# Kernel tuning notes

Measured on AMD Instinct MI355X. Metric: run time of the kernel, lower is better.

## Reference

```python
import jax, jax.numpy as jnp
import numpy as np

D, H, S, T, NN, IN_CH, FEAT, SPA, OUT, NL, FF, E = 512, 8, 64, 32, 512, 32, 64, 32, 32, 4, 2048, 16384
NEG = 0.2  # leaky relu negative slope (GATv2 default and alpha)

def _ln(x, g, b):
    m = x.mean(-1, keepdims=True)
    v = ((x - m) ** 2).mean(-1, keepdims=True)
    return (x - m) / jnp.sqrt(v + 1e-5) * g + b

def _posenc(L):
    pos = jnp.arange(L, dtype=jnp.float32)[:, None]
    div = jnp.exp(-jnp.log(10000.0) * jnp.arange(0, D, 2, dtype=jnp.float32) / D)
    pe = jnp.zeros((L, D), jnp.float32)
    pe = pe.at[:, 0::2].set(jnp.sin(pos * div)).at[:, 1::2].set(jnp.cos(pos * div))
    return pe[:, None, :]  # (L,1,D), seq-first

def _mha(xq, xkv, wqkv, bqkv, wo, bo, mask=None):
    Lq, N, _ = xq.shape
    Lk = xkv.shape[0]
    dh = D // H
    wq, wk, wv = jnp.split(wqkv, 3, axis=1)
    bq, bk, bv = jnp.split(bqkv, 3)
    q = (xq @ wq + bq).reshape(Lq, N, H, dh)
    k = (xkv @ wk + bk).reshape(Lk, N, H, dh)
    v = (xkv @ wv + bv).reshape(Lk, N, H, dh)
    s = jnp.einsum('qnhd,knhd->nhqk', q, k) / jnp.sqrt(jnp.float32(dh))
    if mask is not None:
        s = s + mask
    a = jax.nn.softmax(s, -1)
    o = jnp.einsum('nhqk,knhd->qnhd', a, v).reshape(Lq, N, D)
    return o @ wo + bo

def _gatv2(x, wl, wr, bl, br, att, bias, e_src, e_dst):
    # GATv2: e_ij = a . leakyrelu(Wl x_j + Wr x_i); softmax over incoming edges of i; out_i = sum alpha_ij Wl x_j
    n = x.shape[0]
    h, c = att.shape
    xl = (x @ wl + bl).reshape(n, h, c)
    xr = (x @ wr + br).reshape(n, h, c)
    z = jax.nn.leaky_relu(xl[e_src] + xr[e_dst], NEG)   # (E,H,C)
    e = jnp.einsum('ehc,hc->eh', z, att)                # (E,H)
    m = jax.lax.stop_gradient(jax.ops.segment_max(e, e_dst, num_segments=n))
    ex = jnp.exp(e - m[e_dst])
    den = jax.ops.segment_sum(ex, e_dst, num_segments=n)
    alpha = ex / den[e_dst]
    out = jax.ops.segment_sum(alpha[..., None] * xl[e_src], e_dst, num_segments=n)
    return out.reshape(n, h * c) + bias

def _fwd(src, tgt, w_enc_in, b_enc_in, w_dec_in, b_dec_in, w_map, b_map,
         enc_qkv_w, enc_qkv_b, enc_out_w, enc_out_b, enc_ff1_w, enc_ff1_b, enc_ff2_w, enc_ff2_b,
         enc_ln1_g, enc_ln1_b, enc_ln2_g, enc_ln2_b, enc_fn_g, enc_fn_b,
         dec_sa_qkv_w, dec_sa_qkv_b, dec_sa_out_w, dec_sa_out_b,
         dec_ca_qkv_w, dec_ca_qkv_b, dec_ca_out_w, dec_ca_out_b,
         dec_ff1_w, dec_ff1_b, dec_ff2_w, dec_ff2_b,
         dec_ln1_g, dec_ln1_b, dec_ln2_g, dec_ln2_b, dec_ln3_g, dec_ln3_b, dec_fn_g, dec_fn_b,
         g1_wl, g1_wr, g1_bl, g1_br, g1_att, g1_bias,
         g2_wl, g2_wr, g2_bl, g2_br, g2_att, g2_bias,
         edge_index):
    # temporal transformer (eval mode, dropout off), seq-first (L, N, D)
    x = src @ w_enc_in + b_enc_in + _posenc(S)
    for i in range(NL):  # post-norm encoder, relu FFN (nn.TransformerEncoderLayer defaults)
        a = _mha(x, x, enc_qkv_w[i], enc_qkv_b[i], enc_out_w[i], enc_out_b[i])
        x = _ln(x + a, enc_ln1_g[i], enc_ln1_b[i])
        f = jax.nn.relu(x @ enc_ff1_w[i] + enc_ff1_b[i]) @ enc_ff2_w[i] + enc_ff2_b[i]
        x = _ln(x + f, enc_ln2_g[i], enc_ln2_b[i])
    mem = _ln(x, enc_fn_g, enc_fn_b)
    causal = jnp.triu(jnp.full((T, T), -1e9, jnp.float32), k=1)
    y = tgt @ w_dec_in + b_dec_in + _posenc(T)
    for i in range(NL):
        a = _mha(y, y, dec_sa_qkv_w[i], dec_sa_qkv_b[i], dec_sa_out_w[i], dec_sa_out_b[i], causal)
        y = _ln(y + a, dec_ln1_g[i], dec_ln1_b[i])
        a = _mha(y, mem, dec_ca_qkv_w[i], dec_ca_qkv_b[i], dec_ca_out_w[i], dec_ca_out_b[i])
        y = _ln(y + a, dec_ln2_g[i], dec_ln2_b[i])
        f = jax.nn.relu(y @ dec_ff1_w[i] + dec_ff1_b[i]) @ dec_ff2_w[i] + dec_ff2_b[i]
        y = _ln(y + f, dec_ln3_g[i], dec_ln3_b[i])
    y = _ln(y, dec_fn_g, dec_fn_b) @ w_map + b_map  # (T, N, FEAT)
    e_src, e_dst = edge_index[0], edge_index[1]
    def spatial(xt):  # two-layer GATv2 per time step, then elu (concat=True branch)
        h1 = _gatv2(xt, g1_wl, g1_wr, g1_bl, g1_br, g1_att, g1_bias, e_src, e_dst)
        h2 = _gatv2(h1, g2_wl, g2_wr, g2_bl, g2_br, g2_att, g2_bias, e_src, e_dst)
        return jax.nn.elu(h2)
    g = jax.vmap(spatial)(y)  # (T, N, H*OUT)
    return jax.nn.relu(g)


def setup_inputs():
    ks = iter(jax.random.split(jax.random.key(0), 100))
    def w(shape, s=0.05):
        return jax.random.normal(next(ks), shape, jnp.float32) * s
    inp = {}
    inp['src'] = jax.random.normal(next(ks), (S, NN, IN_CH), jnp.float32)
    inp['tgt'] = jax.random.normal(next(ks), (T, NN, FEAT), jnp.float32)
    inp['w_enc_in'] = w((IN_CH, D)); inp['b_enc_in'] = jnp.zeros((D,))
    inp['w_dec_in'] = w((FEAT, D)); inp['b_dec_in'] = jnp.zeros((D,))
    inp['w_map'] = w((D, FEAT)); inp['b_map'] = jnp.zeros((FEAT,))
    inp['enc_qkv_w'] = w((NL, D, 3 * D)); inp['enc_qkv_b'] = jnp.zeros((NL, 3 * D))
    inp['enc_out_w'] = w((NL, D, D)); inp['enc_out_b'] = jnp.zeros((NL, D))
    inp['enc_ff1_w'] = w((NL, D, FF)); inp['enc_ff1_b'] = jnp.zeros((NL, FF))
    inp['enc_ff2_w'] = w((NL, FF, D)); inp['enc_ff2_b'] = jnp.zeros((NL, D))
    inp['enc_ln1_g'] = jnp.ones((NL, D)); inp['enc_ln1_b'] = jnp.zeros((NL, D))
    inp['enc_ln2_g'] = jnp.ones((NL, D)); inp['enc_ln2_b'] = jnp.zeros((NL, D))
    inp['enc_fn_g'] = jnp.ones((D,)); inp['enc_fn_b'] = jnp.zeros((D,))
    inp['dec_sa_qkv_w'] = w((NL, D, 3 * D)); inp['dec_sa_qkv_b'] = jnp.zeros((NL, 3 * D))
    inp['dec_sa_out_w'] = w((NL, D, D)); inp['dec_sa_out_b'] = jnp.zeros((NL, D))
    inp['dec_ca_qkv_w'] = w((NL, D, 3 * D)); inp['dec_ca_qkv_b'] = jnp.zeros((NL, 3 * D))
    inp['dec_ca_out_w'] = w((NL, D, D)); inp['dec_ca_out_b'] = jnp.zeros((NL, D))
    inp['dec_ff1_w'] = w((NL, D, FF)); inp['dec_ff1_b'] = jnp.zeros((NL, FF))
    inp['dec_ff2_w'] = w((NL, FF, D)); inp['dec_ff2_b'] = jnp.zeros((NL, D))
    inp['dec_ln1_g'] = jnp.ones((NL, D)); inp['dec_ln1_b'] = jnp.zeros((NL, D))
    inp['dec_ln2_g'] = jnp.ones((NL, D)); inp['dec_ln2_b'] = jnp.zeros((NL, D))
    inp['dec_ln3_g'] = jnp.ones((NL, D)); inp['dec_ln3_b'] = jnp.zeros((NL, D))
    inp['dec_fn_g'] = jnp.ones((D,)); inp['dec_fn_b'] = jnp.zeros((D,))
    inp['g1_wl'] = w((FEAT, H * SPA)); inp['g1_wr'] = w((FEAT, H * SPA))
    inp['g1_bl'] = jnp.zeros((H * SPA,)); inp['g1_br'] = jnp.zeros((H * SPA,))
    inp['g1_att'] = w((H, SPA), 0.1); inp['g1_bias'] = jnp.zeros((H * SPA,))
    inp['g2_wl'] = w((H * SPA, H * OUT)); inp['g2_wr'] = w((H * SPA, H * OUT))
    inp['g2_bl'] = jnp.zeros((H * OUT,)); inp['g2_br'] = jnp.zeros((H * OUT,))
    inp['g2_att'] = w((H, OUT), 0.1); inp['g2_bias'] = jnp.zeros((H * OUT,))
    inp['edge_index'] = jax.random.randint(next(ks), (2, E), 0, NN)
    return inp


def reference(src, tgt, w_enc_in, b_enc_in, w_dec_in, b_dec_in, w_map, b_map,
              enc_qkv_w, enc_qkv_b, enc_out_w, enc_out_b, enc_ff1_w, enc_ff1_b, enc_ff2_w, enc_ff2_b,
              enc_ln1_g, enc_ln1_b, enc_ln2_g, enc_ln2_b, enc_fn_g, enc_fn_b,
              dec_sa_qkv_w, dec_sa_qkv_b, dec_sa_out_w, dec_sa_out_b,
              dec_ca_qkv_w, dec_ca_qkv_b, dec_ca_out_w, dec_ca_out_b,
              dec_ff1_w, dec_ff1_b, dec_ff2_w, dec_ff2_b,
              dec_ln1_g, dec_ln1_b, dec_ln2_g, dec_ln2_b, dec_ln3_g, dec_ln3_b, dec_fn_g, dec_fn_b,
              g1_wl, g1_wr, g1_bl, g1_br, g1_att, g1_bias,
              g2_wl, g2_wr, g2_bl, g2_br, g2_att, g2_bias,
              edge_index):
    return _fwd(src, tgt, w_enc_in, b_enc_in, w_dec_in, b_dec_in, w_map, b_map,
                enc_qkv_w, enc_qkv_b, enc_out_w, enc_out_b, enc_ff1_w, enc_ff1_b, enc_ff2_w, enc_ff2_b,
                enc_ln1_g, enc_ln1_b, enc_ln2_g, enc_ln2_b, enc_fn_g, enc_fn_b,
                dec_sa_qkv_w, dec_sa_qkv_b, dec_sa_out_w, dec_sa_out_b,
                dec_ca_qkv_w, dec_ca_qkv_b, dec_ca_out_w, dec_ca_out_b,
                dec_ff1_w, dec_ff1_b, dec_ff2_w, dec_ff2_b,
                dec_ln1_g, dec_ln1_b, dec_ln2_g, dec_ln2_b, dec_ln3_g, dec_ln3_b, dec_fn_g, dec_fn_b,
                g1_wl, g1_wr, g1_bl, g1_br, g1_att, g1_bias,
                g2_wl, g2_wr, g2_bl, g2_br, g2_att, g2_bias,
                edge_index)
```

## Files before the change

### kernel.cpp

```cpp
#include <hip/hip_runtime.h>
#include <hip/hip_bf16.h>

#define NHEAD 8
#define SLEN 64
#define TLEN 32
#define NNODE 512
#define NEDGE 16384
#define NLAYER 4

typedef __attribute__((ext_vector_type(8))) __bf16 bf16x8;
typedef __attribute__((ext_vector_type(4))) __bf16 bf16x4;
typedef __attribute__((ext_vector_type(4))) float  f32x4;

__device__ __forceinline__ void gload16(const void* g, void* l)
{
    __builtin_amdgcn_global_load_lds(
        (const __attribute__((address_space(1))) void*)g,
        (__attribute__((address_space(3))) void*)l, 16, 0, 0);
}

template<int BN>
__global__ __launch_bounds__(256) void gemm_bf16(
    const __bf16* __restrict__ A, int lda,
    const __bf16* __restrict__ Bt, int ldb,
    const float* __restrict__ bias,
    const __bf16* __restrict__ Res,
    float* __restrict__ Cf, __bf16* __restrict__ Cb, int ldc,
    int M, int N, int K, int outMode)
{
    constexpr int FM = (BN == 128) ? 4 : 2;
    __shared__ __bf16 As[128 * 64];
    __shared__ __bf16 Bs[BN * 64];
    const int tid  = threadIdx.x;
    const int wid  = tid >> 6;
    const int lane = tid & 63;
    const int wr = (BN == 128) ? (wid >> 1) : wid;
    const int wc = (BN == 128) ? (wid & 1) : 0;
    const int m0 = blockIdx.y * 128, n0 = blockIdx.x * BN;

    const int srow = wid * 8 + (lane >> 3);
    const int scol = (lane & 7) * 8;
    const int lr = lane & 15;
    const int kg = (lane >> 4) * 8;

    f32x4 acc[FM][4];
    #pragma unroll
    for (int m = 0; m < FM; ++m)
        #pragma unroll
        for (int n = 0; n < 4; ++n)
            acc[m][n] = (f32x4){0.0f, 0.0f, 0.0f, 0.0f};

    for (int k0 = 0; k0 < K; k0 += 64) {
        #pragma unroll
        for (int g = 0; g < 4; ++g) {
            const __bf16* ga = A + (size_t)(m0 + g * 32 + srow) * lda + k0 + scol;
            gload16(ga, &As[(g * 32 + wid * 8) * 64]);
        }
        #pragma unroll
        for (int g = 0; g < BN / 32; ++g) {
            const __bf16* gb = Bt + (size_t)(n0 + g * 32 + srow) * ldb + k0 + scol;
            gload16(gb, &Bs[(g * 32 + wid * 8) * 64]);
        }
        __syncthreads();
        #pragma unroll
        for (int kk = 0; kk < 64; kk += 32) {
            bf16x8 fa[FM], fb[4];
            #pragma unroll
            for (int m = 0; m < FM; ++m)
                fa[m] = *reinterpret_cast<const bf16x8*>(
                    &As[(wr * (16 * FM) + m * 16 + lr) * 64 + kk + kg]);
            #pragma unroll
            for (int n = 0; n < 4; ++n)
                fb[n] = *reinterpret_cast<const bf16x8*>(
                    &Bs[(wc * 64 + n * 16 + lr) * 64 + kk + kg]);
            #pragma unroll
            for (int m = 0; m < FM; ++m)
                #pragma unroll
                for (int n = 0; n < 4; ++n)
                    acc[m][n] = __builtin_amdgcn_mfma_f32_16x16x32_bf16(
                        fa[m], fb[n], acc[m][n], 0, 0, 0);
        }
        __syncthreads();
    }

    const int cr = (lane >> 4) * 4;
    const int cc = lane & 15;
    #pragma unroll
    for (int n = 0; n < 4; ++n) {
        const int gcol = n0 + wc * 64 + n * 16 + cc;
        const float bb = bias[gcol];
        #pragma unroll
        for (int m = 0; m < FM; ++m) {
            #pragma unroll
            for (int j = 0; j < 4; ++j) {
                const int grow = m0 + wr * (16 * FM) + m * 16 + cr + j;
                float v = acc[m][n][j] + bb;
                if (Res) v += (float)Res[(size_t)grow * ldc + gcol];
                if (outMode == 1 || outMode == 2) v = fmaxf(v, 0.0f);
                if (outMode >= 2) Cb[(size_t)grow * ldc + gcol] = (__bf16)v;
                else              Cf[(size_t)grow * ldc + gcol] = v;
            }
        }
    }
}

__global__ __launch_bounds__(256) void gemm_bias(
    const float* __restrict__ A, int lda,
    const float* __restrict__ B, int ldb,
    const float* __restrict__ bias,
    float* __restrict__ C, int ldc,
    int M, int N, int K, int relu)
{
    __shared__ float As[16][68];
    __shared__ float Bs[16][68];
    const int tid = threadIdx.x;
    const int tx = tid & 15, ty = tid >> 4;
    const int m0 = blockIdx.y * 64, n0 = blockIdx.x * 64;
    const int liA_m = tid >> 2;
    const int liA_k = (tid & 3) * 4;
    const int liB_n = (tid & 15) * 4;
    const int liB_k = tid >> 4;
    float acc[4][4] = {};
    for (int k0 = 0; k0 < K; k0 += 16) {
        float4 av = *reinterpret_cast<const float4*>(&A[(size_t)(m0 + liA_m) * lda + k0 + liA_k]);
        float4 bv = *reinterpret_cast<const float4*>(&B[(size_t)(k0 + liB_k) * ldb + n0 + liB_n]);
        As[liA_k + 0][liA_m] = av.x;
        As[liA_k + 1][liA_m] = av.y;
        As[liA_k + 2][liA_m] = av.z;
        As[liA_k + 3][liA_m] = av.w;
        *reinterpret_cast<float4*>(&Bs[liB_k][liB_n]) = bv;
        __syncthreads();
        #pragma unroll
        for (int kk = 0; kk < 16; ++kk) {
            float4 a4 = *reinterpret_cast<const float4*>(&As[kk][ty * 4]);
            float4 b4 = *reinterpret_cast<const float4*>(&Bs[kk][tx * 4]);
            float a[4] = {a4.x, a4.y, a4.z, a4.w};
            float b[4] = {b4.x, b4.y, b4.z, b4.w};
            #pragma unroll
            for (int i = 0; i < 4; ++i)
                #pragma unroll
                for (int j = 0; j < 4; ++j)
                    acc[i][j] += a[i] * b[j];
        }
        __syncthreads();
    }
    #pragma unroll
    for (int i = 0; i < 4; ++i) {
        const int m = m0 + ty * 4 + i;
        #pragma unroll
        for (int j = 0; j < 4; ++j) {
            const int n = n0 + tx * 4 + j;
            float v = acc[i][j] + bias[n];
            if (relu) v = fmaxf(v, 0.0f);
            C[(size_t)m * ldc + n] = v;
        }
    }
}

__global__ __launch_bounds__(256) void transpose_w(
    const float* __restrict__ in, __bf16* __restrict__ out, int K, int N)
{
    __shared__ __bf16 t[32][33];
    const int l = blockIdx.z;
    in  += (size_t)l * K * N;
    out += (size_t)l * K * N;
    const int k0 = blockIdx.y * 32, n0 = blockIdx.x * 32;
    const int tx = threadIdx.x & 31, ty = threadIdx.x >> 5;
    #pragma unroll
    for (int i = 0; i < 32; i += 8)
        t[ty + i][tx] = (__bf16)in[(size_t)(k0 + ty + i) * N + n0 + tx];
    __syncthreads();
    #pragma unroll
    for (int i = 0; i < 32; i += 8)
        out[(size_t)(n0 + ty + i) * K + k0 + tx] = t[tx][ty + i];
}

__global__ __launch_bounds__(256) void conv_bf16(
    const float* __restrict__ in, __bf16* __restrict__ out, int total4)
{
    const int i = blockIdx.x * 256 + threadIdx.x;
    if (i >= total4) return;
    const float4 v = *reinterpret_cast<const float4*>(&in[(size_t)i * 4]);
    bf16x4 w;
    w[0] = (__bf16)v.x; w[1] = (__bf16)v.y; w[2] = (__bf16)v.z; w[3] = (__bf16)v.w;
    *reinterpret_cast<bf16x4*>(&out[(size_t)i * 4]) = w;
}

__global__ __launch_bounds__(256) void permute_in(
    const float* __restrict__ in, float* __restrict__ out, int L, int CH, int total)
{
    const int idx = blockIdx.x * 256 + threadIdx.x;
    if (idx >= total) return;
    const int c = idx % CH;
    const int r = idx / CH;
    const int n = r & 511;
    const int l = r >> 9;
    out[((size_t)n * L + l) * CH + c] = in[idx];
}

__global__ __launch_bounds__(256) void permute_F(
    const __bf16* __restrict__ in, __bf16* __restrict__ out)
{
    const int idx = blockIdx.x * 256 + threadIdx.x;
    if (idx >= 16384 * 64) return;
    const int c = idx & 63;
    const int r = idx >> 6;
    const int n = r >> 5;
    const int t = r & 31;
    out[((size_t)(t * 512 + n)) * 64 + c] = in[idx];
}

template<int LQ, int LK, bool CAUSAL>
__global__ __launch_bounds__(64) void attn_mfma(
    const __bf16* __restrict__ Q, int ldq,
    const __bf16* __restrict__ Kp, int ldk,
    const __bf16* __restrict__ Vp, int ldv,
    __bf16* __restrict__ O, int ldo)
{
    constexpr int QF = LQ / 16, KF = LK / 16;
    constexpr int PSTR = LK + 8;
    __shared__ __bf16 Vt[64 * PSTR];
    __shared__ __bf16 Ps[LQ * PSTR];
    const int n = blockIdx.x >> 3;
    const int h = blockIdx.x & 7;
    const int lane = threadIdx.x;
    const int lr = lane & 15;
    const int g4 = lane >> 4;
    const int kg = g4 * 8;

    if (lane < LK) {
        #pragma unroll
        for (int j = 0; j < 8; ++j) {
            bf16x8 vv = *reinterpret_cast<const bf16x8*>(
                &Vp[(size_t)(n * LK + lane) * ldv + h * 64 + j * 8]);
            #pragma unroll
            for (int e = 0; e < 8; ++e)
                Vt[(j * 8 + e) * PSTR + lane] = vv[e];
        }
    }

    f32x4 s[QF][KF];
    #pragma unroll
    for (int qi = 0; qi < QF; ++qi)
        #pragma unroll
        for (int ki = 0; ki < KF; ++ki)
            s[qi][ki] = (f32x4){0.0f, 0.0f, 0.0f, 0.0f};
    #pragma unroll
    for (int kk = 0; kk < 64; kk += 32) {
        bf16x8 fa[QF], fb[KF];
        #pragma unroll
        for (int qi = 0; qi < QF; ++qi)
            fa[qi] = *reinterpret_cast<const bf16x8*>(
                &Q[(size_t)(n * LQ + qi * 16 + lr) * ldq + h * 64 + kk + kg]);
        #pragma unroll
        for (int ki = 0; ki < KF; ++ki)
            fb[ki] = *reinterpret_cast<const bf16x8*>(
                &Kp[(size_t)(n * LK + ki * 16 + lr) * ldk + h * 64 + kk + kg]);
        #pragma unroll
        for (int qi = 0; qi < QF; ++qi)
            #pragma unroll
            for (int ki = 0; ki < KF; ++ki)
                s[qi][ki] = __builtin_amdgcn_mfma_f32_16x16x32_bf16(fa[qi], fb[ki], s[qi][ki], 0, 0, 0);
    }

    float inv_s[QF][4];
    #pragma unroll
    for (int qi = 0; qi < QF; ++qi) {
        #pragma unroll
        for (int j = 0; j < 4; ++j) {
            const int row = qi * 16 + g4 * 4 + j;
            float mx = -1e30f;
            #pragma unroll
            for (int ki = 0; ki < KF; ++ki) {
                float v = s[qi][ki][j] * 0.125f;
                if (CAUSAL) { const int col = ki * 16 + lr; if (col > row) v = -1e30f; }
                s[qi][ki][j] = v;
                mx = fmaxf(mx, v);
            }
            #pragma unroll
            for (int d = 1; d < 16; d <<= 1) mx = fmaxf(mx, __shfl_xor(mx, d));
            float sum = 0.0f;
            #pragma unroll
            for (int ki = 0; ki < KF; ++ki) {
                const float p = __expf(s[qi][ki][j] - mx);
                s[qi][ki][j] = p;
                sum += p;
            }
            #pragma unroll
            for (int d = 1; d < 16; d <<= 1) sum += __shfl_xor(sum, d);
            inv_s[qi][j] = 1.0f / sum;
            #pragma unroll
            for (int ki = 0; ki < KF; ++ki)
                Ps[row * PSTR + ki * 16 + lr] = (__bf16)s[qi][ki][j];
        }
    }
    __syncthreads();

    f32x4 o[QF][4];
    #pragma unroll
    for (int qi = 0; qi < QF; ++qi)
        #pragma unroll
        for (int di = 0; di < 4; ++di)
            o[qi][di] = (f32x4){0.0f, 0.0f, 0.0f, 0.0f};
    #pragma unroll
    for (int kk = 0; kk < LK; kk += 32) {
        bf16x8 fa[QF], fb[4];
        #pragma unroll
        for (int qi = 0; qi < QF; ++qi)
            fa[qi] = *reinterpret_cast<const bf16x8*>(&Ps[(qi * 16 + lr) * PSTR + kk + kg]);
        #pragma unroll
        for (int di = 0; di < 4; ++di)
            fb[di] = *reinterpret_cast<const bf16x8*>(&Vt[(di * 16 + lr) * PSTR + kk + kg]);
        #pragma unroll
        for (int qi = 0; qi < QF; ++qi)
            #pragma unroll
            for (int di = 0; di < 4; ++di)
                o[qi][di] = __builtin_amdgcn_mfma_f32_16x16x32_bf16(fa[qi], fb[di], o[qi][di], 0, 0, 0);
    }
    #pragma unroll
    for (int qi = 0; qi < QF; ++qi)
        #pragma unroll
        for (int di = 0; di < 4; ++di)
            #pragma unroll
            for (int j = 0; j < 4; ++j) {
                const int row = qi * 16 + g4 * 4 + j;
                O[(size_t)(n * LQ + row) * ldo + h * 64 + di * 16 + lr] =
                    (__bf16)(o[qi][di][j] * inv_s[qi][j]);
            }
}

template<bool HASR, bool F32OUT>
__global__ __launch_bounds__(256) void ln_bf16(
    const __bf16* __restrict__ X, const __bf16* __restrict__ Rb,
    const float* __restrict__ g, const float* __restrict__ b,
    __bf16* __restrict__ outb, float* __restrict__ outf, int ntok)
{
    const int wid = threadIdx.x >> 6, lane = threadIdx.x & 63;
    const int row = blockIdx.x * 4 + wid;
    if (row >= ntok) return;
    const size_t base = (size_t)row * 512;
    const int c0 = lane * 8;
    const bf16x8 xv = *reinterpret_cast<const bf16x8*>(&X[base + c0]);
    float v[8];
    float s = 0.0f;
    if (HASR) {
        const bf16x8 rv = *reinterpret_cast<const bf16x8*>(&Rb[base + c0]);
        #pragma unroll
        for (int j = 0; j < 8; ++j) { v[j] = (float)xv[j] + (float)rv[j]; s += v[j]; }
    } else {
        #pragma unroll
        for (int j = 0; j < 8; ++j) { v[j] = (float)xv[j]; s += v[j]; }
    }
    #pragma unroll
    for (int d = 32; d >= 1; d >>= 1) s += __shfl_xor(s, d, 64);
    const float mean = s * (1.0f / 512.0f);
    float vs = 0.0f;
    #pragma unroll
    for (int j = 0; j < 8; ++j) { const float d = v[j] - mean; vs += d * d; }
    #pragma unroll
    for (int d = 32; d >= 1; d >>= 1) vs += __shfl_xor(vs, d, 64);
    const float rstd = rsqrtf(vs * (1.0f / 512.0f) + 1e-5f);
    const float4 g0 = *reinterpret_cast<const float4*>(&g[c0]);
    const float4 g1 = *reinterpret_cast<const float4*>(&g[c0 + 4]);
    const float4 b0 = *reinterpret_cast<const float4*>(&b[c0]);
    const float4 b1 = *reinterpret_cast<const float4*>(&b[c0 + 4]);
    const float gg[8] = {g0.x, g0.y, g0.z, g0.w, g1.x, g1.y, g1.z, g1.w};
    const float bb[8] = {b0.x, b0.y, b0.z, b0.w, b1.x, b1.y, b1.z, b1.w};
    if (F32OUT) {
        f32x4 o0, o1;
        #pragma unroll
        for (int j = 0; j < 4; ++j) o0[j] = (v[j] - mean) * rstd * gg[j] + bb[j];
        #pragma unroll
        for (int j = 0; j < 4; ++j) o1[j] = (v[4 + j] - mean) * rstd * gg[4 + j] + bb[4 + j];
        *reinterpret_cast<f32x4*>(&outf[base + c0]) = o0;
        *reinterpret_cast<f32x4*>(&outf[base + c0 + 4]) = o1;
    } else {
        bf16x8 w;
        #pragma unroll
        for (int j = 0; j < 8; ++j) w[j] = (__bf16)((v[j] - mean) * rstd * gg[j] + bb[j]);
        *reinterpret_cast<bf16x8*>(&outb[base + c0]) = w;
    }
}

__global__ __launch_bounds__(256) void add_posenc(float* __restrict__ x, int L, int total)
{
    const int idx = blockIdx.x * 256 + threadIdx.x;
    if (idx >= total) return;
    const int d = idx & 511;
    const int row = idx >> 9;
    const int l = row % L;
    const int i2 = d & ~1;
    const float freq = expf(-9.210340371976184f * (float)i2 / 512.0f);
    const float a = (float)l * freq;
    x[idx] += (d & 1) ? cosf(a) : sinf(a);
}

__global__ void zero_ints(int* __restrict__ p, int n)
{
    const int i = blockIdx.x * 256 + threadIdx.x;
    if (i < n) p[i] = 0;
}

__global__ void count_deg(const int* __restrict__ edst, int* __restrict__ deg)
{
    const int e = blockIdx.x * 256 + threadIdx.x;
    if (e < NEDGE) atomicAdd(&deg[edst[e]], 1);
}

__global__ void scan512(const int* __restrict__ deg, int* __restrict__ off)
{
    __shared__ int s[512];
    const int tid = threadIdx.x;
    s[tid] = deg[tid];
    __syncthreads();
    for (int d = 1; d < 512; d <<= 1) {
        const int t = (tid >= d) ? s[tid - d] : 0;
        __syncthreads();
        s[tid] += t;
        __syncthreads();
    }
    off[tid + 1] = s[tid];
    if (tid == 0) off[0] = 0;
}

__global__ void fill_eid(const int* __restrict__ edst, const int* __restrict__ off,
                         int* __restrict__ cur, int* __restrict__ eid)
{
    const int e = blockIdx.x * 256 + threadIdx.x;
    if (e < NEDGE) {
        const int d = edst[e];
        const int pos = off[d] + atomicAdd(&cur[d], 1);
        eid[pos] = e;
    }
}

template<bool FINAL>
__global__ __launch_bounds__(256) void gatv2_kernel(
    const float* __restrict__ xl, const float* __restrict__ xr,
    const float* __restrict__ att, const float* __restrict__ bias,
    const int* __restrict__ off, const int* __restrict__ eid,
    const int* __restrict__ esrc,
    __bf16* __restrict__ outb16, float* __restrict__ outd)
{
    const int blk = blockIdx.x;
    const int i = blk & (NNODE - 1);
    const int t = blk >> 9;
    const int tid = threadIdx.x;
    const float xrv = xr[(size_t)blk * 256 + tid];
    const float av = att[tid];
    const int e0 = off[i], e1 = off[i + 1];
    float m = -1e30f, den = 0.0f, acc = 0.0f;
    for (int base = e0; base < e1; base += 16) {
        float xv[16], ws[16];
        float tm = -1e30f;
        #pragma unroll
        for (int k = 0; k < 16; ++k) {
            const int idx = base + k;
            float w = -1e30f, xlv = 0.0f;
            if (idx < e1) {
                const int s = esrc[eid[idx]];
                xlv = xl[((size_t)(t * 512 + s)) * 256 + tid];
                float z = xlv + xrv;
                z = (z > 0.0f) ? z : 0.2f * z;
                w = z * av;
                #pragma unroll
                for (int d = 16; d >= 1; d >>= 1) w += __shfl_xor(w, d, 32);
            }
            ws[k] = w;
            xv[k] = xlv;
            tm = fmaxf(tm, w);
        }
        const float mn = fmaxf(m, tm);
        const float sc = __expf(m - mn);
        den *= sc; acc *= sc; m = mn;
        #pragma unroll
        for (int k = 0; k < 16; ++k) {
            const float p = __expf(ws[k] - m);
            den += p;
            acc += p * xv[k];
        }
    }
    float o = (den > 0.0f) ? acc / den : 0.0f;
    o += bias[tid];
    if (FINAL) {
        o = fmaxf(o, 0.0f);
        outd[(size_t)blk * 256 + tid] = o;
    } else {
        outb16[(size_t)blk * 256 + tid] = (__bf16)o;
    }
}

extern "C" void kernel_launch(void* const* d_in, const int* in_sizes, int n_in,
                              void* d_out, int out_size, void* d_ws, size_t ws_size,
                              hipStream_t stream)
{
    const float* src       = (const float*)d_in[0];
    const float* tgt       = (const float*)d_in[1];
    const float* w_enc_in  = (const float*)d_in[2];
    const float* b_enc_in  = (const float*)d_in[3];
    const float* w_dec_in  = (const float*)d_in[4];
    const float* b_dec_in  = (const float*)d_in[5];
    const float* w_map     = (const float*)d_in[6];
    const float* b_map     = (const float*)d_in[7];
    const float* enc_qkv_w = (const float*)d_in[8];
    const float* enc_qkv_b = (const float*)d_in[9];
    const float* enc_out_w = (const float*)d_in[10];
    const float* enc_out_b = (const float*)d_in[11];
    const float* enc_ff1_w = (const float*)d_in[12];
    const float* enc_ff1_b = (const float*)d_in[13];
    const float* enc_ff2_w = (const float*)d_in[14];
    const float* enc_ff2_b = (const float*)d_in[15];
    const float* enc_ln1_g = (const float*)d_in[16];
    const float* enc_ln1_b = (const float*)d_in[17];
    const float* enc_ln2_g = (const float*)d_in[18];
    const float* enc_ln2_b = (const float*)d_in[19];
    const float* enc_fn_g  = (const float*)d_in[20];
    const float* enc_fn_b  = (const float*)d_in[21];
    const float* dec_sa_qkv_w = (const float*)d_in[22];
    const float* dec_sa_qkv_b = (const float*)d_in[23];
    const float* dec_sa_out_w = (const float*)d_in[24];
    const float* dec_sa_out_b = (const float*)d_in[25];
    const float* dec_ca_qkv_w = (const float*)d_in[26];
    const float* dec_ca_qkv_b = (const float*)d_in[27];
    const float* dec_ca_out_w = (const float*)d_in[28];
    const float* dec_ca_out_b = (const float*)d_in[29];
    const float* dec_ff1_w = (const float*)d_in[30];
    const float* dec_ff1_b = (const float*)d_in[31];
    const float* dec_ff2_w = (const float*)d_in[32];
    const float* dec_ff2_b = (const float*)d_in[33];
    const float* dec_ln1_g = (const float*)d_in[34];
    const float* dec_ln1_b = (const float*)d_in[35];
    const float* dec_ln2_g = (const float*)d_in[36];
    const float* dec_ln2_b = (const float*)d_in[37];
    const float* dec_ln3_g = (const float*)d_in[38];
    const float* dec_ln3_b = (const float*)d_in[39];
    const float* dec_fn_g  = (const float*)d_in[40];
    const float* dec_fn_b  = (const float*)d_in[41];
    const float* g1_wl   = (const float*)d_in[42];
    const float* g1_wr   = (const float*)d_in[43];
    const float* g1_bl   = (const float*)d_in[44];
    const float* g1_br   = (const float*)d_in[45];
    const float* g1_att  = (const float*)d_in[46];
    const float* g1_bias = (const float*)d_in[47];
    const float* g2_wl   = (const float*)d_in[48];
    const float* g2_wr   = (const float*)d_in[49];
    const float* g2_bl   = (const float*)d_in[50];
    const float* g2_br   = (const float*)d_in[51];
    const float* g2_att  = (const float*)d_in[52];
    const float* g2_bias = (const float*)d_in[53];
    const int*   edge_index = (const int*)d_in[54];
    const int* esrc = edge_index;
    const int* edst = edge_index + NEDGE;

    float* wsf = (float*)d_ws;
    __bf16* Xb = (__bf16*)wsf;
    __bf16* Yb = (__bf16*)(wsf + 8388608);
    float*  Rf = wsf + 12582912;
    float*  Mf = wsf + 20971520;
    float*  Wf = wsf + 29360128;
    float*  F  = wsf + 37748736;
    int* ipool = (int*)(wsf + 38797312);
    int* deg = ipool;
    int* off = deg + 512;
    int* cur = off + 516;
    int* eid = cur + 512;
    __bf16* Rb16 = (__bf16*)Rf;
    __bf16* Mb16 = (__bf16*)Mf;
    __bf16* Wb   = (__bf16*)Wf;

    auto gemm = [&](const float* A, int lda, const float* B, int ldb, const float* bias,
                    float* Cc, int ldc, int M, int N, int K, int relu) {
        dim3 grid((unsigned)(N / 64), (unsigned)(M / 64));
        gemm_bias<<<grid, 256, 0, stream>>>(A, lda, B, ldb, bias, Cc, ldc, M, N, K, relu);
    };
    auto gemmT = [&](const __bf16* A, int lda, const __bf16* Bt, int ldb,
                     const float* bias, float* Cf, __bf16* Cb, int ldc,
                     int M, int N, int K, int mode) {
        dim3 grid((unsigned)(N / 128), (unsigned)(M / 128));
        gemm_bf16<128><<<grid, 256, 0, stream>>>(A, lda, Bt, ldb, bias, nullptr, Cf, Cb, ldc, M, N, K, mode);
    };
    auto gemmT64 = [&](const __bf16* A, int lda, const __bf16* Bt, int ldb,
                       const float* bias, float* Cf, __bf16* Cb, int ldc,
                       int M, int N, int K, int mode) {
        dim3 grid((unsigned)(N / 64), (unsigned)(M / 128));
        gemm_bf16<64><<<grid, 256, 0, stream>>>(A, lda, Bt, ldb, bias, nullptr, Cf, Cb, ldc, M, N, K, mode);
    };
    auto tw = [&](const float* w, __bf16* o, int K, int N, int L) {
        dim3 g((unsigned)(N / 32), (unsigned)(K / 32), (unsigned)L);
        transpose_w<<<g, 256, 0, stream>>>(w, o, K, N);
    };

    zero_ints<<<8, 256, 0, stream>>>(ipool, 512 + 516 + 512);
    count_deg<<<NEDGE / 256, 256, 0, stream>>>(edst, deg);
    scan512<<<1, 512, 0, stream>>>(deg, off);
    fill_eid<<<NEDGE / 256, 256, 0, stream>>>(edst, off, cur, eid);

    {
        float* src_nm = Wf;
        float* Xtmp = Rf;
        permute_in<<<4096, 256, 0, stream>>>(src, src_nm, SLEN, 32, 32768 * 32);
        gemm(src_nm, 32, w_enc_in, 512, b_enc_in, Xtmp, 512, 32768, 512, 32, 0);
        add_posenc<<<(32768 * 512) / 256, 256, 0, stream>>>(Xtmp, SLEN, 32768 * 512);
        conv_bf16<<<16384, 256, 0, stream>>>(Xtmp, Xb, 32768 * 128);
        float* tgt_nm = Wf;
        float* Ytmp = Rf;
        permute_in<<<4096, 256, 0, stream>>>(tgt, tgt_nm, TLEN, 64, 16384 * 64);
        gemm(tgt_nm, 64, w_dec_in, 512, b_dec_in, Ytmp, 512, 16384, 512, 64, 0);
        add_posenc<<<(16384 * 512) / 256, 256, 0, stream>>>(Ytmp, TLEN, 16384 * 512);
        conv_bf16<<<8192, 256, 0, stream>>>(Ytmp, Yb, 16384 * 128);
    }

    __bf16* WeQkv = Wb + 0;
    __bf16* WeOut = Wb + 3145728;
    __bf16* WeFf1 = Wb + 4194304;
    __bf16* WeFf2 = Wb + 8388608;
    tw(enc_qkv_w, WeQkv, 512, 1536, NLAYER);
    tw(enc_out_w, WeOut, 512, 512, NLAYER);
    tw(enc_ff1_w, WeFf1, 512, 2048, NLAYER);
    tw(enc_ff2_w, WeFf2, 2048, 512, NLAYER);

    for (int i = 0; i < NLAYER; ++i) {
        for (int c = 0; c < 4; ++c) {
            gemmT(Xb + (size_t)c * 8192 * 512, 512, WeQkv + (size_t)i * 786432, 512,
                  enc_qkv_b + (size_t)i * 1536, nullptr, Rb16, 1536, 8192, 1536, 512, 3);
            attn_mfma<64, 64, false><<<1024, 64, 0, stream>>>(
                Rb16, 1536, Rb16 + 512, 1536, Rb16 + 1024, 1536,
                Mb16 + (size_t)c * 8192 * 512, 512);
        }
        gemmT(Mb16, 512, WeOut + (size_t)i * 262144, 512, enc_out_b + (size_t)i * 512,
              nullptr, Rb16, 512, 32768, 512, 512, 3);
        ln_bf16<true, false><<<8192, 256, 0, stream>>>(Xb, Rb16,
            enc_ln1_g + (size_t)i * 512, enc_ln1_b + (size_t)i * 512, Xb, nullptr, 32768);
        for (int s = 0; s < 4; ++s) {
            gemmT(Xb + (size_t)s * 8192 * 512, 512, WeFf1 + (size_t)i * 1048576, 512,
                  enc_ff1_b + (size_t)i * 2048, nullptr, Mb16, 2048, 8192, 2048, 512, 2);
            gemmT64(Mb16, 2048, WeFf2 + (size_t)i * 1048576, 2048,
                    enc_ff2_b + (size_t)i * 512, nullptr, Rb16 + (size_t)s * 8192 * 512, 512,
                    8192, 512, 2048, 3);
        }
        ln_bf16<true, false><<<8192, 256, 0, stream>>>(Xb, Rb16,
            enc_ln2_g + (size_t)i * 512, enc_ln2_b + (size_t)i * 512, Xb, nullptr, 32768);
    }
    ln_bf16<false, false><<<8192, 256, 0, stream>>>(Xb, nullptr, enc_fn_g, enc_fn_b,
                                                    Xb, nullptr, 32768);

    __bf16* WdSaQkv = Wb + 0;
    __bf16* WdSaOut = Wb + 3145728;
    __bf16* WdCaQkv = Wb + 4194304;
    __bf16* WdCaOut = Wb + 7340032;
    __bf16* WdFf1   = Wb + 8388608;
    __bf16* WdFf2   = Wb + 12582912;
    tw(dec_sa_qkv_w, WdSaQkv, 512, 1536, NLAYER);
    tw(dec_sa_out_w, WdSaOut, 512, 512, NLAYER);
    tw(dec_ca_qkv_w, WdCaQkv, 512, 1536, NLAYER);
    tw(dec_ca_out_w, WdCaOut, 512, 512, NLAYER);
    tw(dec_ff1_w,    WdFf1,   512, 2048, NLAYER);
    tw(dec_ff2_w,    WdFf2,   2048, 512, NLAYER);

    __bf16* ObD  = Mb16;
    __bf16* QbC  = Mb16;
    __bf16* ObCA = (__bf16*)(Mf + 2097152);
    for (int i = 0; i < NLAYER; ++i) {
        for (int c = 0; c < 2; ++c) {
            gemmT(Yb + (size_t)c * 8192 * 512, 512, WdSaQkv + (size_t)i * 786432, 512,
                  dec_sa_qkv_b + (size_t)i * 1536, nullptr, Rb16, 1536, 8192, 1536, 512, 3);
            attn_mfma<32, 32, true><<<2048, 64, 0, stream>>>(
                Rb16, 1536, Rb16 + 512, 1536, Rb16 + 1024, 1536,
                ObD + (size_t)c * 8192 * 512, 512);
        }
        gemmT64(ObD, 512, WdSaOut + (size_t)i * 262144, 512, dec_sa_out_b + (size_t)i * 512,
                nullptr, Rb16, 512, 16384, 512, 512, 3);
        ln_bf16<true, false><<<4096, 256, 0, stream>>>(Yb, Rb16,
            dec_ln1_g + (size_t)i * 512, dec_ln1_b + (size_t)i * 512, Yb, nullptr, 16384);
        for (int c = 0; c < 2; ++c) {
            gemmT64(Yb + (size_t)c * 8192 * 512, 512, WdCaQkv + (size_t)i * 786432, 512,
                    dec_ca_qkv_b + (size_t)i * 1536, nullptr, QbC, 512, 8192, 512, 512, 3);
            gemmT(Xb + (size_t)c * 16384 * 512, 512, WdCaQkv + (size_t)i * 786432 + 262144, 512,
                  dec_ca_qkv_b + (size_t)i * 1536 + 512, nullptr, Rb16, 1024, 16384, 1024, 512, 3);
            attn_mfma<32, 64, false><<<2048, 64, 0, stream>>>(
                QbC, 512, Rb16, 1024, Rb16 + 512, 1024,
                ObCA + (size_t)c * 8192 * 512, 512);
        }
        gemmT64(ObCA, 512, WdCaOut + (size_t)i * 262144, 512, dec_ca_out_b + (size_t)i * 512,
                nullptr, Rb16, 512, 16384, 512, 512, 3);
        ln_bf16<true, false><<<4096, 256, 0, stream>>>(Yb, Rb16,
            dec_ln2_g + (size_t)i * 512, dec_ln2_b + (size_t)i * 512, Yb, nullptr, 16384);
        for (int s = 0; s < 2; ++s) {
            gemmT(Yb + (size_t)s * 8192 * 512, 512, WdFf1 + (size_t)i * 1048576, 512,
                  dec_ff1_b + (size_t)i * 2048, nullptr, Mb16, 2048, 8192, 2048, 512, 2);
            gemmT64(Mb16, 2048, WdFf2 + (size_t)i * 1048576, 2048,
                    dec_ff2_b + (size_t)i * 512, nullptr, Rb16 + (size_t)s * 8192 * 512, 512,
                    8192, 512, 2048, 3);
        }
        ln_bf16<true, false><<<4096, 256, 0, stream>>>(Yb, Rb16,
            dec_ln3_g + (size_t)i * 512, dec_ln3_b + (size_t)i * 512, Yb, nullptr, 16384);
    }
    ln_bf16<false, false><<<4096, 256, 0, stream>>>(Yb, nullptr, dec_fn_g, dec_fn_b,
                                                    Yb, nullptr, 16384);

    __bf16* Wmapt = Wb;
    __bf16* G1wlT = Wb + 32768;
    __bf16* G1wrT = Wb + 49152;
    __bf16* G2wlT = Wb + 65536;
    __bf16* G2wrT = Wb + 131072;
    __bf16* Ftb   = Wb + 196608;
    __bf16* Ibb   = Wb + 1245184;
    tw(w_map, Wmapt, 512, 64, 1);
    tw(g1_wl, G1wlT, 64, 256, 1);
    tw(g1_wr, G1wrT, 64, 256, 1);
    tw(g2_wl, G2wlT, 256, 256, 1);
    tw(g2_wr, G2wrT, 256, 256, 1);

    __bf16* Fb16 = (__bf16*)F;
    gemmT64(Yb, 512, Wmapt, 512, b_map, nullptr, Fb16, 64, 16384, 64, 512, 3);
    permute_F<<<4096, 256, 0, stream>>>(Fb16, Ftb);

    float* G  = Mf;
    float* Hb = Mf + 4194304;
    gemmT64(Ftb, 64, G1wlT, 64, g1_bl, G,  nullptr, 256, 16384, 256, 64, 0);
    gemmT64(Ftb, 64, G1wrT, 64, g1_br, Hb, nullptr, 256, 16384, 256, 64, 0);
    gatv2_kernel<false><<<16384, 256, 0, stream>>>(G, Hb, g1_att, g1_bias, off, eid, esrc,
                                                   Ibb, nullptr);
    gemmT64(Ibb, 256, G2wlT, 256, g2_bl, G,  nullptr, 256, 16384, 256, 256, 0);
    gemmT64(Ibb, 256, G2wrT, 256, g2_br, Hb, nullptr, 256, 16384, 256, 256, 0);
    gatv2_kernel<true><<<16384, 256, 0, stream>>>(G, Hb, g2_att, g2_bias, off, eid, esrc,
                                                  nullptr, (float*)d_out);
}
```

Before: 4.766 ms.

## Fuse input projection with posenc, batch cross-attn Q GEMM, revert GAT chunking

Fuses the input projection GEMM, the positional encoding add and the bf16 conversion into one kernel. This removes two elementwise passes and an fp32 intermediate buffer. Cross-attention Q projection now runs as one GEMM over all 16384 rows instead of two chunked launches, which requires moving the ObCA buffer offset. It also adds s_setprio around MFMA blocks in attention, drops the unused residual path in the GEMM, and replaces the chunked 16-edge GAT loop with a simpler per-edge online softmax, which may reduce memory-level parallelism.

```diff
diff --git a/kernel.cpp b/kernel.cpp
--- a/kernel.cpp
+++ b/kernel.cpp
@@ -24,7 +24,6 @@
     const __bf16* __restrict__ A, int lda,
     const __bf16* __restrict__ Bt, int ldb,
     const float* __restrict__ bias,
-    const __bf16* __restrict__ Res,
     float* __restrict__ Cf, __bf16* __restrict__ Cb, int ldc,
     int M, int N, int K, int outMode)
 {
@@ -95,7 +94,6 @@
             for (int j = 0; j < 4; ++j) {
                 const int grow = m0 + wr * (16 * FM) + m * 16 + cr + j;
                 float v = acc[m][n][j] + bb;
-                if (Res) v += (float)Res[(size_t)grow * ldc + gcol];
                 if (outMode == 1 || outMode == 2) v = fmaxf(v, 0.0f);
                 if (outMode >= 2) Cb[(size_t)grow * ldc + gcol] = (__bf16)v;
                 else              Cf[(size_t)grow * ldc + gcol] = v;
@@ -104,12 +102,12 @@
     }
 }
 
-__global__ __launch_bounds__(256) void gemm_bias(
+__global__ __launch_bounds__(256) void gemm_in_pe(
     const float* __restrict__ A, int lda,
     const float* __restrict__ B, int ldb,
     const float* __restrict__ bias,
-    float* __restrict__ C, int ldc,
-    int M, int N, int K, int relu)
+    __bf16* __restrict__ Cb, int ldc,
+    int M, int N, int K, int posencL)
 {
     __shared__ float As[16][68];
     __shared__ float Bs[16][68];
@@ -147,12 +145,16 @@
     #pragma unroll
     for (int i = 0; i < 4; ++i) {
         const int m = m0 + ty * 4 + i;
+        const int l = m % posencL;
         #pragma unroll
         for (int j = 0; j < 4; ++j) {
             const int n = n0 + tx * 4 + j;
             float v = acc[i][j] + bias[n];
-            if (relu) v = fmaxf(v, 0.0f);
-            C[(size_t)m * ldc + n] = v;
+            const int i2 = n & ~1;
+            const float freq = __expf(-9.210340371976184f * (float)i2 / 512.0f);
+            const float a = (float)l * freq;
+            v += (n & 1) ? __cosf(a) : __sinf(a);
+            Cb[(size_t)m * ldc + n] = (__bf16)v;
         }
     }
 }
@@ -173,17 +175,6 @@
     #pragma unroll
     for (int i = 0; i < 32; i += 8)
         out[(size_t)(n0 + ty + i) * K + k0 + tx] = t[tx][ty + i];
-}
-
-__global__ __launch_bounds__(256) void conv_bf16(
-    const float* __restrict__ in, __bf16* __restrict__ out, int total4)
-{
-    const int i = blockIdx.x * 256 + threadIdx.x;
-    if (i >= total4) return;
-    const float4 v = *reinterpret_cast<const float4*>(&in[(size_t)i * 4]);
-    bf16x4 w;
-    w[0] = (__bf16)v.x; w[1] = (__bf16)v.y; w[2] = (__bf16)v.z; w[3] = (__bf16)v.w;
-    *reinterpret_cast<bf16x4*>(&out[(size_t)i * 4]) = w;
 }
 
 __global__ __launch_bounds__(256) void permute_in(
@@ -256,11 +247,13 @@
         for (int ki = 0; ki < KF; ++ki)
             fb[ki] = *reinterpret_cast<const bf16x8*>(
                 &Kp[(size_t)(n * LK + ki * 16 + lr) * ldk + h * 64 + kk + kg]);
+        __builtin_amdgcn_s_setprio(1);
         #pragma unroll
         for (int qi = 0; qi < QF; ++qi)
             #pragma unroll
             for (int ki = 0; ki < KF; ++ki)
                 s[qi][ki] = __builtin_amdgcn_mfma_f32_16x16x32_bf16(fa[qi], fb[ki], s[qi][ki], 0, 0, 0);
+        __builtin_amdgcn_s_setprio(0);
     }
 
     float inv_s[QF][4];
@@ -311,11 +304,13 @@
         #pragma unroll
         for (int di = 0; di < 4; ++di)
             fb[di] = *reinterpret_cast<const bf16x8*>(&Vt[(di * 16 + lr) * PSTR + kk + kg]);
+        __builtin_amdgcn_s_setprio(1);
         #pragma unroll
         for (int qi = 0; qi < QF; ++qi)
             #pragma unroll
             for (int di = 0; di < 4; ++di)
                 o[qi][di] = __builtin_amdgcn_mfma_f32_16x16x32_bf16(fa[qi], fb[di], o[qi][di], 0, 0, 0);
+        __builtin_amdgcn_s_setprio(0);
     }
     #pragma unroll
     for (int qi = 0; qi < QF; ++qi)
@@ -382,19 +377,6 @@
     }
 }
 
-__global__ __launch_bounds__(256) void add_posenc(float* __restrict__ x, int L, int total)
-{
-    const int idx = blockIdx.x * 256 + threadIdx.x;
-    if (idx >= total) return;
-    const int d = idx & 511;
-    const int row = idx >> 9;
-    const int l = row % L;
-    const int i2 = d & ~1;
-    const float freq = expf(-9.210340371976184f * (float)i2 / 512.0f);
-    const float a = (float)l * freq;
-    x[idx] += (d & 1) ? cosf(a) : sinf(a);
-}
-
 __global__ void zero_ints(int* __restrict__ p, int n)
 {
     const int i = blockIdx.x * 256 + threadIdx.x;
@@ -450,35 +432,21 @@
     const float av = att[tid];
     const int e0 = off[i], e1 = off[i + 1];
     float m = -1e30f, den = 0.0f, acc = 0.0f;
-    for (int base = e0; base < e1; base += 16) {
-        float xv[16], ws[16];
-        float tm = -1e30f;
-        #pragma unroll
-        for (int k = 0; k < 16; ++k) {
-            const int idx = base + k;
-            float w = -1e30f, xlv = 0.0f;
-            if (idx < e1) {
-                const int s = esrc[eid[idx]];
-                xlv = xl[((size_t)(t * 512 + s)) * 256 + tid];
-                float z = xlv + xrv;
-                z = (z > 0.0f) ? z : 0.2f * z;
-                w = z * av;
-                #pragma unroll
-                for (int d = 16; d >= 1; d >>= 1) w += __shfl_xor(w, d, 32);
-            }
-            ws[k] = w;
-            xv[k] = xlv;
-            tm = fmaxf(tm, w);
-        }
-        const float mn = fmaxf(m, tm);
+    for (int idx = e0; idx < e1; ++idx) {
+        const int e = eid[idx];
+        const int s = esrc[e];
+        const float xlv = xl[((size_t)(t * 512 + s)) * 256 + tid];
+        float z = xlv + xrv;
+        z = (z > 0.0f) ? z : 0.2f * z;
+        float w = z * av;
+        #pragma unroll
+        for (int d = 16; d >= 1; d >>= 1) w += __shfl_xor(w, d, 32);
+        const float mn = fmaxf(m, w);
         const float sc = __expf(m - mn);
-        den *= sc; acc *= sc; m = mn;
-        #pragma unroll
-        for (int k = 0; k < 16; ++k) {
-            const float p = __expf(ws[k] - m);
-            den += p;
-            acc += p * xv[k];
-        }
+        const float p  = __expf(w - mn);
+        den = den * sc + p;
+        acc = acc * sc + p * xlv;
+        m = mn;
     }
     float o = (den > 0.0f) ? acc / den : 0.0f;
     o += bias[tid];
@@ -568,22 +536,17 @@
     __bf16* Mb16 = (__bf16*)Mf;
     __bf16* Wb   = (__bf16*)Wf;
 
-    auto gemm = [&](const float* A, int lda, const float* B, int ldb, const float* bias,
-                    float* Cc, int ldc, int M, int N, int K, int relu) {
-        dim3 grid((unsigned)(N / 64), (unsigned)(M / 64));
-        gemm_bias<<<grid, 256, 0, stream>>>(A, lda, B, ldb, bias, Cc, ldc, M, N, K, relu);
-    };
     auto gemmT = [&](const __bf16* A, int lda, const __bf16* Bt, int ldb,
                      const float* bias, float* Cf, __bf16* Cb, int ldc,
                      int M, int N, int K, int mode) {
         dim3 grid((unsigned)(N / 128), (unsigned)(M / 128));
-        gemm_bf16<128><<<grid, 256, 0, stream>>>(A, lda, Bt, ldb, bias, nullptr, Cf, Cb, ldc, M, N, K, mode);
+        gemm_bf16<128><<<grid, 256, 0, stream>>>(A, lda, Bt, ldb, bias, Cf, Cb, ldc, M, N, K, mode);
     };
     auto gemmT64 = [&](const __bf16* A, int lda, const __bf16* Bt, int ldb,
                        const float* bias, float* Cf, __bf16* Cb, int ldc,
                        int M, int N, int K, int mode) {
         dim3 grid((unsigned)(N / 64), (unsigned)(M / 128));
-        gemm_bf16<64><<<grid, 256, 0, stream>>>(A, lda, Bt, ldb, bias, nullptr, Cf, Cb, ldc, M, N, K, mode);
+        gemm_bf16<64><<<grid, 256, 0, stream>>>(A, lda, Bt, ldb, bias, Cf, Cb, ldc, M, N, K, mode);
     };
     auto tw = [&](const float* w, __bf16* o, int K, int N, int L) {
         dim3 g((unsigned)(N / 32), (unsigned)(K / 32), (unsigned)L);
@@ -597,17 +560,13 @@
 
     {
         float* src_nm = Wf;
-        float* Xtmp = Rf;
         permute_in<<<4096, 256, 0, stream>>>(src, src_nm, SLEN, 32, 32768 * 32);
-        gemm(src_nm, 32, w_enc_in, 512, b_enc_in, Xtmp, 512, 32768, 512, 32, 0);
-        add_posenc<<<(32768 * 512) / 256, 256, 0, stream>>>(Xtmp, SLEN, 32768 * 512);
-        conv_bf16<<<16384, 256, 0, stream>>>(Xtmp, Xb, 32768 * 128);
+        gemm_in_pe<<<dim3(8, 512), 256, 0, stream>>>(src_nm, 32, w_enc_in, 512,
+                                                     b_enc_in, Xb, 512, 32768, 512, 32, SLEN);
         float* tgt_nm = Wf;
-        float* Ytmp = Rf;
         permute_in<<<4096, 256, 0, stream>>>(tgt, tgt_nm, TLEN, 64, 16384 * 64);
-        gemm(tgt_nm, 64, w_dec_in, 512, b_dec_in, Ytmp, 512, 16384, 512, 64, 0);
-        add_posenc<<<(16384 * 512) / 256, 256, 0, stream>>>(Ytmp, TLEN, 16384 * 512);
-        conv_bf16<<<8192, 256, 0, stream>>>(Ytmp, Yb, 16384 * 128);
+        gemm_in_pe<<<dim3(8, 256), 256, 0, stream>>>(tgt_nm, 64, w_dec_in, 512,
+                                                     b_dec_in, Yb, 512, 16384, 512, 64, TLEN);
     }
 
     __bf16* WeQkv = Wb + 0;
@@ -659,7 +618,7 @@
 
     __bf16* ObD  = Mb16;
     __bf16* QbC  = Mb16;
-    __bf16* ObCA = (__bf16*)(Mf + 2097152);
+    __bf16* ObCA = (__bf16*)(Mf + 4194304);
     for (int i = 0; i < NLAYER; ++i) {
         for (int c = 0; c < 2; ++c) {
             gemmT(Yb + (size_t)c * 8192 * 512, 512, WdSaQkv + (size_t)i * 786432, 512,
@@ -672,13 +631,13 @@
                 nullptr, Rb16, 512, 16384, 512, 512, 3);
         ln_bf16<true, false><<<4096, 256, 0, stream>>>(Yb, Rb16,
             dec_ln1_g + (size_t)i * 512, dec_ln1_b + (size_t)i * 512, Yb, nullptr, 16384);
+        gemmT64(Yb, 512, WdCaQkv + (size_t)i * 786432, 512,
+                dec_ca_qkv_b + (size_t)i * 1536, nullptr, QbC, 512, 16384, 512, 512, 3);
         for (int c = 0; c < 2; ++c) {
-            gemmT64(Yb + (size_t)c * 8192 * 512, 512, WdCaQkv + (size_t)i * 786432, 512,
-                    dec_ca_qkv_b + (size_t)i * 1536, nullptr, QbC, 512, 8192, 512, 512, 3);
             gemmT(Xb + (size_t)c * 16384 * 512, 512, WdCaQkv + (size_t)i * 786432 + 262144, 512,
                   dec_ca_qkv_b + (size_t)i * 1536 + 512, nullptr, Rb16, 1024, 16384, 1024, 512, 3);
             attn_mfma<32, 64, false><<<2048, 64, 0, stream>>>(
-                QbC, 512, Rb16, 1024, Rb16 + 512, 1024,
+                QbC + (size_t)c * 8192 * 512, 512, Rb16, 1024, Rb16 + 512, 1024,
                 ObCA + (size_t)c * 8192 * 512, 512);
         }
         gemmT64(ObCA, 512, WdCaOut + (size_t)i * 262144, 512, dec_ca_out_b + (size_t)i * 512,
```

New measurement: 4.534 ms. 1.05x faster.
